# Optimization experiments

Hardware: AMD Instinct MI355X
Metric: run time of the kernel (lower is better)

The kernel has to match this reference:

```python
import jax, jax.numpy as jnp
import numpy as np
from jax import lax

# NOTE: ResidualConvBlock and SS2DChanelFirst are reconstructed from the repo's
# conventions: ResidualConvBlock = act(conv3x3 -> act -> conv3x3 + 1x1 skip);
# SS2DChanelFirst = standard VMamba SS2D (in_proj -> dw-conv3x3 -> SiLU ->
# 4-direction cross-scan selective scan -> cross-merge -> LayerNorm -> *SiLU(z)
# gate -> out_proj) operating on NCHW tensors.

B, CIN, H, W = 4, 6, 64, 64
DM, DI, K, N, R, NL, GROUPS = 72, 144, 4, 8, 4, 2, 12


def conv2d(x, w, b=None, groups=1):
    out = lax.conv_general_dilated(x, w, (1, 1), 'SAME',
                                   dimension_numbers=('NCHW', 'OIHW', 'NCHW'),
                                   feature_group_count=groups)
    if b is not None:
        out = out + b[None, :, None, None]
    return out


def lrelu(x, s):
    return jnp.where(x >= 0, x, s * x)


def selective_scan(u, delta, A, Bs, Cs, D):
    # u, delta: (b,K,C,L); A: (K,C,N); Bs, Cs: (b,K,N,L); D: (K,C)
    b, k, c, l = u.shape
    n = A.shape[-1]
    ul = jnp.moveaxis(u, -1, 0)
    dl = jnp.moveaxis(delta, -1, 0)
    Bl = jnp.moveaxis(Bs, -1, 0)
    Cl = jnp.moveaxis(Cs, -1, 0)
    h0 = jnp.zeros((b, k, c, n), u.dtype)

    def step(h, xt):
        d_t, u_t, B_t, C_t = xt
        h = h * jnp.exp(d_t[..., None] * A) + (d_t * u_t)[..., None] * B_t[:, :, None, :]
        return h, jnp.einsum('bkcn,bkn->bkc', h, C_t)

    _, ys = lax.scan(step, h0, (dl, ul, Bl, Cl))
    return jnp.moveaxis(ys, 0, -1) + u * D[None, :, :, None]


def ss2d(x, in_w, dw_w, dw_b, xp_w, dtp_w, dtp_b, A_logs, Ds, ong, onb, op_w):
    b, dm, h_, w_ = x.shape
    l = h_ * w_
    xz = jnp.einsum('ec,bchw->behw', in_w, x)  # (b, 2*DI, h, w)
    xi, z = xz[:, :DI], xz[:, DI:]
    xi = jax.nn.silu(conv2d(xi, dw_w, dw_b, groups=DI))
    # cross-scan: row-major, col-major, and their reverses
    x0 = xi.reshape(b, DI, l)
    x1 = jnp.swapaxes(xi, 2, 3).reshape(b, DI, l)
    xs = jnp.stack([x0, x1, x0[..., ::-1], x1[..., ::-1]], axis=1)  # (b,4,DI,l)
    x_dbl = jnp.einsum('bkdl,kcd->bkcl', xs, xp_w)  # (b,4,R+2N,l)
    dts, Bs, Cs = x_dbl[:, :, :R], x_dbl[:, :, R:R + N], x_dbl[:, :, R + N:]
    dts = jnp.einsum('bkrl,kdr->bkdl', dts, dtp_w)
    delta = jax.nn.softplus(dts + dtp_b[None, :, :, None])
    A = -jnp.exp(A_logs).reshape(K, DI, N)
    ys = selective_scan(xs, delta, A, Bs, Cs, Ds.reshape(K, DI))  # (b,4,DI,l)
    # cross-merge
    y = ys[:, 0] + ys[:, 2, :, ::-1]
    yt = ys[:, 1] + ys[:, 3, :, ::-1]
    y = y + jnp.swapaxes(yt.reshape(b, DI, w_, h_), 2, 3).reshape(b, DI, l)
    y = jnp.swapaxes(y, 1, 2)  # (b,l,DI)
    mu = y.mean(-1, keepdims=True)
    var = ((y - mu) ** 2).mean(-1, keepdims=True)
    y = (y - mu) / jnp.sqrt(var + 1e-5) * ong + onb
    y = y * jax.nn.silu(jnp.swapaxes(z.reshape(b, DI, l), 1, 2))
    out = jnp.einsum('bld,ed->ble', y, op_w)  # (b,l,DM)
    return jnp.swapaxes(out, 1, 2).reshape(b, dm, h_, w_)


def groupnorm(x, g, bta, groups):
    b, c, h_, w_ = x.shape
    xg = x.reshape(b, groups, c // groups, h_ * w_)
    mu = xg.mean((2, 3), keepdims=True)
    var = ((xg - mu) ** 2).mean((2, 3), keepdims=True)
    xg = (xg - mu) / jnp.sqrt(var + 1e-5)
    return xg.reshape(b, c, h_, w_) * g[None, :, None, None] + bta[None, :, None, None]


def setup_inputs() -> dict:
    key = jax.random.key(0)
    ks = iter(jax.random.split(key, 32))
    nrm = lambda shp, s=0.05: jax.random.normal(next(ks), shp, jnp.float32) * s
    inp = {
        'image': jax.random.normal(next(ks), (B, CIN, H, W), jnp.float32),
        'cb_w1': nrm((DM, CIN, 3, 3), 0.1), 'cb_b1': nrm((DM,), 0.02),
        'cb_w2': nrm((DM, DM, 3, 3), 0.05), 'cb_b2': nrm((DM,), 0.02),
        'cb_ws': nrm((DM, CIN, 1, 1), 0.1), 'cb_bs': nrm((DM,), 0.02),
        'in_w': nrm((NL, 2 * DI, DM), 0.05),
        'dw_w': nrm((NL, DI, 1, 3, 3), 0.1), 'dw_b': nrm((NL, DI), 0.02),
        'xp_w': nrm((NL, K, R + 2 * N, DI), 0.05),
        'dtp_w': nrm((NL, K, DI, R), 0.1), 'dtp_b': nrm((NL, K, DI), 0.1),
        'A_logs': nrm((NL, K * DI, N), 0.5),
        'Ds': jnp.ones((NL, K * DI), jnp.float32) + nrm((NL, K * DI), 0.05),
        'ong': jnp.ones((NL, DI), jnp.float32), 'onb': jnp.zeros((NL, DI), jnp.float32),
        'op_w': nrm((NL, DM, DI), 0.05),
        'gn_g': jnp.ones((NL, DM), jnp.float32), 'gn_b': jnp.zeros((NL, DM), jnp.float32),
        'l1_w': nrm((NL, DM, DM), 0.1), 'l1_b': nrm((NL, DM), 0.02),
        'l2_w': nrm((NL, DM, DM), 0.1), 'l2_b': nrm((NL, DM), 0.02),
        'shrink_w': nrm((CIN, DM, 3, 3), 0.05), 'shrink_b': nrm((CIN,), 0.02),
    }
    return inp


def reference(image, cb_w1, cb_b1, cb_w2, cb_b2, cb_ws, cb_bs, in_w, dw_w, dw_b,
              xp_w, dtp_w, dtp_b, A_logs, Ds, ong, onb, op_w, gn_g, gn_b,
              l1_w, l1_b, l2_w, l2_b, shrink_w, shrink_b):
    # ResidualConvBlock (expand 6 -> 72), leaky_relu
    h = lrelu(conv2d(image, cb_w1, cb_b1), 0.01)
    h = conv2d(h, cb_w2, cb_b2) + conv2d(image, cb_ws, cb_bs)
    x = lrelu(h, 0.01)
    for i in range(NL):
        x = ss2d(x, in_w[i], dw_w[i], dw_b[i], xp_w[i], dtp_w[i], dtp_b[i],
                 A_logs[i], Ds[i], ong[i], onb[i], op_w[i])
        x = groupnorm(x, gn_g[i], gn_b[i], GROUPS)
        x = jnp.einsum('oc,bchw->bohw', l1_w[i], x) + l1_b[i][None, :, None, None]
        x = lrelu(x, 0.04)
        x = jnp.einsum('oc,bchw->bohw', l2_w[i], x) + l2_b[i][None, :, None, None]
    x = conv2d(x, shrink_w, shrink_b)
    return jax.nn.sigmoid(x)
```

## Files before the change

kernel.cpp:

```cpp
#include <hip/hip_runtime.h>
#include <math.h>

#define BB 4
#define CI 6
#define LL 4096
#define DMC 72
#define DIC 144
#define KD 4
#define NS 8
#define RD 4
#define NLAYER 2
#define GRP 12
#define NCH 256
#define TS 16
#define PP 4356
#define L2E 1.4426950408889634f

__device__ __forceinline__ float sigmoidf_(float x){ return 1.f/(1.f+__expf(-x)); }
__device__ __forceinline__ float siluf_(float x){ return x*sigmoidf_(x); }
__device__ __forceinline__ float softplusf_(float x){
  return fmaxf(x,0.f) + __logf(1.f + __expf(-fabsf(x)));
}

__device__ __forceinline__ int padidx(int p){ return 66*(p>>6) + (p&63) + 67; }

__device__ __forceinline__ int dirmap(int k, int l){
  switch(k & 3){
    case 0: return l;
    case 1: return ((l & 63) << 6) | (l >> 6);
    case 2: return (LL-1) - l;
    default: { int m = (LL-1) - l; return ((m & 63) << 6) | (m >> 6); }
  }
}

#define LOAD9(ip, a) do { \
  a[0]=(ip)[-67]; a[1]=(ip)[-66]; a[2]=(ip)[-65]; \
  a[3]=(ip)[-1];  a[4]=(ip)[0];   a[5]=(ip)[1];   \
  a[6]=(ip)[65];  a[7]=(ip)[66];  a[8]=(ip)[67];  } while(0)

__global__ void k_halo(float* __restrict__ pads, int nplanes){
  int plane = blockIdx.x;
  if (plane >= nplanes) return;
  int t = threadIdx.x;
  if (t >= 260) return;
  float* pl = pads + (size_t)plane*PP;
  int off;
  if (t < 132){
    int row = (t < 66) ? 0 : 65;
    int col = (t < 66) ? t : t-66;
    off = row*66 + col;
  } else {
    int j = t - 132;
    int col = (j < 64) ? 0 : 65;
    int row = 1 + (j & 63);
    off = row*66 + col;
  }
  pl[off] = 0.f;
}

__global__ void k_pad_img(const float* __restrict__ img, float* __restrict__ img_pad){
  int idx = blockIdx.x*256 + threadIdx.x;
  if (idx >= BB*CI*LL) return;
  int p = idx & 4095; int bc = idx >> 12;
  img_pad[(size_t)bc*PP + padidx(p)] = img[idx];
}

__global__ void k_conv1(const float* __restrict__ img_pad, const float* __restrict__ w,
                        const float* __restrict__ bias, float* __restrict__ tmp_pad){
  int bid = blockIdx.x;
  int t = bid & 15; int r = bid >> 4; int o = r % DMC; int b = r / DMC;
  int p = t*256 + threadIdx.x;
  int pb = padidx(p);
  float acc = bias[o];
  const float* wb = w + o*CI*9;
  #pragma unroll
  for (int ic=0; ic<CI; ++ic){
    const float* ip = img_pad + (size_t)(b*CI+ic)*PP + pb;
    float a[9]; LOAD9(ip, a);
    #pragma unroll
    for (int q=0;q<9;++q) acc += a[q]*wb[ic*9+q];
  }
  tmp_pad[(size_t)(b*DMC+o)*PP + pb] = acc >= 0.f ? acc : 0.01f*acc;
}

__global__ void k_conv2init(const float* __restrict__ img, const float* __restrict__ b2,
                            const float* __restrict__ wsc, const float* __restrict__ bsc,
                            float* __restrict__ xout){
  int bid = blockIdx.x;
  int t = bid & 15; int r = bid >> 4; int og = r % 18; int b = r / 18;
  int p = t*256 + threadIdx.x;
  float acc[4];
  #pragma unroll
  for (int j=0;j<4;++j) acc[j] = b2[og*4+j] + bsc[og*4+j];
  #pragma unroll
  for (int ic=0; ic<CI; ++ic){
    float v = img[((b*CI+ic)<<12)+p];
    #pragma unroll
    for (int j=0;j<4;++j) acc[j] += v * wsc[(og*4+j)*CI+ic];
  }
  #pragma unroll
  for (int j=0;j<4;++j)
    xout[((b*DMC+og*4+j)<<12)+p] = acc[j];
}

__global__ void k_conv2(const float* __restrict__ tmp_pad,
                        const float* __restrict__ w2, float* __restrict__ xout){
  int bid = blockIdx.x;
  int t = bid & 15; int r = bid >> 4; int og = r % 18; r /= 18;
  int icg = r & 1; int b = r >> 1;
  int p = t*256 + threadIdx.x;
  int pb = padidx(p);
  float acc[4] = {0.f,0.f,0.f,0.f};
  const float* ipb = tmp_pad + (size_t)b*DMC*PP + pb;
  const float* wb  = w2 + (size_t)(og*4)*DMC*9;
  #pragma unroll 2
  for (int ii=0; ii<36; ++ii){
    int ic = icg*36 + ii;
    const float* ip = ipb + (size_t)ic*PP;
    float a[9]; LOAD9(ip, a);
    const float* wp = wb + ic*9;
    #pragma unroll
    for (int j=0;j<4;++j){
      float s = 0.f;
      #pragma unroll
      for (int q=0;q<9;++q) s += a[q]*wp[(size_t)j*DMC*9 + q];
      acc[j] += s;
    }
  }
  #pragma unroll
  for (int j=0;j<4;++j)
    atomicAdd(xout + ((b*DMC+og*4+j)<<12)+p, acc[j]);
}

__global__ void k_xz(const float* __restrict__ x, const float* __restrict__ inw,
                     float* __restrict__ xz_pad, float* __restrict__ z_t, int relu){
  int bid = blockIdx.x;
  int t = bid & 15; int r = bid >> 4; int eg = r % 36; int b = r / 36;
  int p = t*256 + threadIdx.x;
  float acc[8] = {0.f,0.f,0.f,0.f,0.f,0.f,0.f,0.f};
  for (int c0=0; c0<DMC; c0+=4){
    float a[4];
    #pragma unroll
    for (int q=0;q<4;++q) a[q] = x[((b*DMC+c0+q)<<12)+p];
    if (relu){
      #pragma unroll
      for (int q=0;q<4;++q) a[q] = a[q] >= 0.f ? a[q] : 0.01f*a[q];
    }
    #pragma unroll
    for (int j=0;j<8;++j){
      float4 w = *(const float4*)(inw + (eg*8+j)*DMC + c0);
      acc[j] += a[0]*w.x + a[1]*w.y + a[2]*w.z + a[3]*w.w;
    }
  }
  if (eg < 18){
    int pb = padidx(p);
    #pragma unroll
    for (int j=0;j<8;++j) xz_pad[(size_t)(b*DIC+eg*8+j)*PP + pb] = acc[j];
  } else {
    float* zb = z_t + ((size_t)b*LL+p)*DIC + (eg*8-DIC);
    *(float4*)(zb)   = make_float4(acc[0],acc[1],acc[2],acc[3]);
    *(float4*)(zb+4) = make_float4(acc[4],acc[5],acc[6],acc[7]);
  }
}

__global__ void k_dw(const float* __restrict__ xz_pad, const float* __restrict__ dww,
                     const float* __restrict__ dwb, float* __restrict__ xi_t){
  int bid = blockIdx.x;
  int t = bid & 15; int r = bid >> 4; int c = r % DIC; int b = r / DIC;
  int p = t*256 + threadIdx.x;
  int pb = padidx(p);
  const float* ip = xz_pad + (size_t)(b*DIC+c)*PP + pb;
  const float* wp = dww + c*9;
  float a[9]; LOAD9(ip, a);
  float acc = dwb[c];
  #pragma unroll
  for (int q=0;q<9;++q) acc += a[q]*wp[q];
  xi_t[((size_t)b*LL+p)*DIC + c] = siluf_(acc);
}

__global__ void k_xdbl(const float* __restrict__ xi_t, const float* __restrict__ xpw,
                       float* __restrict__ xdbl){
  int bid = blockIdx.x;
  int t = bid & 15; int r = bid >> 4;
  int kk = r & 3; r >>= 2; int part = r & 3; int b = r >> 2;
  int p = t*256 + threadIdx.x;
  const float* xib = xi_t + ((size_t)b*LL + p)*DIC;
  const float* wk = xpw + (size_t)(kk*20 + part*5)*DIC;
  float acc[5] = {0.f,0.f,0.f,0.f,0.f};
  for (int d=0; d<DIC; d+=4){
    float4 v = *(const float4*)(xib + d);
    #pragma unroll
    for (int c=0;c<5;++c){
      float4 w = *(const float4*)(wk + (size_t)c*DIC + d);
      acc[c] += v.x*w.x + v.y*w.y + v.z*w.z + v.w*w.w;
    }
  }
  float* dst = xdbl + ((size_t)(b*KD+kk)*LL + p)*20 + part*5;
  #pragma unroll
  for (int c=0;c<5;++c) dst[c] = acc[c];
}

__device__ __forceinline__ void scan_decode(int idx, int& b, int& k, int& ch, int& c){
  c = idx % DIC;
  int r = idx / DIC;
  ch = r % NCH;
  r /= NCH;
  k = r & 3; b = r >> 2;
}

__global__ void k_p1(const float* __restrict__ xi_t, const float* __restrict__ xdbl,
                     const float* __restrict__ dtpw, const float* __restrict__ dtpb,
                     const float* __restrict__ alog,
                     float* __restrict__ cumA, float* __restrict__ hp){
  int idx = blockIdx.x*256 + threadIdx.x;
  if (idx >= BB*KD*NCH*DIC) return;
  int b,k,ch,c; scan_decode(idx,b,k,ch,c);
  float Arow[NS];
  #pragma unroll
  for (int n=0;n<NS;++n) Arow[n] = -__expf(alog[(k*DIC+c)*NS+n]) * L2E;
  float4 wdt = *(const float4*)(dtpw + (k*DIC+c)*RD);
  float bdt = dtpb[k*DIC+c];
  const float* xd = xdbl + (size_t)(b*KD+k)*LL*20;
  const float* xib = xi_t + (size_t)b*LL*DIC + c;
  float h[NS];
  #pragma unroll
  for (int n=0;n<NS;++n) h[n]=0.f;
  float sumd = 0.f;
  #pragma unroll 4
  for (int t=0; t<TS; ++t){
    int l = ch*TS + t;
    int ps = dirmap(k,l);
    const float* row = xd + (size_t)ps*20;
    float4 q0 = *(const float4*)(row);
    float4 q1 = *(const float4*)(row+4);
    float4 q2 = *(const float4*)(row+8);
    float u = xib[(size_t)ps*DIC];
    float dt = bdt + q0.x*wdt.x + q0.y*wdt.y + q0.z*wdt.z + q0.w*wdt.w;
    dt = softplusf_(dt);
    sumd += dt;
    float du = dt*u;
    float Bv[NS] = {q1.x,q1.y,q1.z,q1.w,q2.x,q2.y,q2.z,q2.w};
    #pragma unroll
    for (int n=0;n<NS;++n)
      h[n] = h[n]*exp2f(dt*Arow[n]) + du*Bv[n];
  }
  size_t base = ((size_t)((b*KD+k)*NCH + ch)*NS)*DIC + c;
  #pragma unroll
  for (int n=0;n<NS;++n) hp[base + n*DIC] = h[n];
  #pragma unroll
  for (int n=0;n<NS;++n) cumA[base + n*DIC] = exp2f(sumd*Arow[n]);
}

__global__ void k_p2(float* __restrict__ cumA, float* __restrict__ hp){
  int idx = blockIdx.x*256 + threadIdx.x;
  if (idx >= BB*KD*NS*DIC) return;
  int c = idx % DIC; int n = (idx/DIC) % NS; int bk = idx/(DIC*NS);
  float h = 0.f;
  #pragma unroll 4
  for (int ch=0; ch<NCH; ++ch){
    size_t base = ((size_t)(bk*NCH+ch)*NS + n)*DIC + c;
    float a = cumA[base];
    float pp = hp[base];
    cumA[base] = 0.f;
    hp[base] = h;
    h = a*h + pp;
  }
}

__global__ void k_p3(const float* __restrict__ xi_t, const float* __restrict__ xdbl,
                     const float* __restrict__ dtpw, const float* __restrict__ dtpb,
                     const float* __restrict__ alog, const float* __restrict__ Dsv,
                     const float* __restrict__ hin, float* __restrict__ y_t){
  int idx = blockIdx.x*256 + threadIdx.x;
  if (idx >= BB*KD*NCH*DIC) return;
  int b,k,ch,c; scan_decode(idx,b,k,ch,c);
  float Arow[NS];
  #pragma unroll
  for (int n=0;n<NS;++n) Arow[n] = -__expf(alog[(k*DIC+c)*NS+n]) * L2E;
  float4 wdt = *(const float4*)(dtpw + (k*DIC+c)*RD);
  float bdt = dtpb[k*DIC+c];
  float Dv = Dsv[k*DIC+c];
  const float* xd = xdbl + (size_t)(b*KD+k)*LL*20;
  const float* xib = xi_t + (size_t)b*LL*DIC + c;
  float* yb = y_t + (size_t)b*LL*DIC + c;
  float h[NS];
  size_t base = ((size_t)((b*KD+k)*NCH + ch)*NS)*DIC + c;
  #pragma unroll
  for (int n=0;n<NS;++n) h[n] = hin[base + n*DIC];
  #pragma unroll 4
  for (int t=0; t<TS; ++t){
    int l = ch*TS + t;
    int ps = dirmap(k,l);
    const float* row = xd + (size_t)ps*20;
    float4 q0 = *(const float4*)(row);
    float4 q1 = *(const float4*)(row+4);
    float4 q2 = *(const float4*)(row+8);
    float4 q3 = *(const float4*)(row+12);
    float4 q4 = *(const float4*)(row+16);
    float u = xib[(size_t)ps*DIC];
    float dt = bdt + q0.x*wdt.x + q0.y*wdt.y + q0.z*wdt.z + q0.w*wdt.w;
    dt = softplusf_(dt);
    float du = dt*u;
    float Bv[NS] = {q1.x,q1.y,q1.z,q1.w,q2.x,q2.y,q2.z,q2.w};
    float Cv[NS] = {q3.x,q3.y,q3.z,q3.w,q4.x,q4.y,q4.z,q4.w};
    float y = 0.f;
    #pragma unroll
    for (int n=0;n<NS;++n){
      h[n] = h[n]*exp2f(dt*Arow[n]) + du*Bv[n];
      y += h[n]*Cv[n];
    }
    y += u*Dv;
    atomicAdd(yb + (size_t)ps*DIC, y);
  }
}

__global__ void k_oproj(const float* __restrict__ y_t, const float* __restrict__ z_t,
                        const float* __restrict__ ong, const float* __restrict__ onb,
                        const float* __restrict__ opw, float* __restrict__ xout,
                        float* __restrict__ gnstats){
  __shared__ float ly[DIC*65];
  __shared__ float red1[8][64], red2[8][64];
  __shared__ float lmu[64], lrs[64];
  int bid = blockIdx.x;
  if (bid == 0 && threadIdx.x < 2*BB*GRP) gnstats[threadIdx.x] = 0.f;
  int tile = bid & 63; int b = bid >> 6;
  int pstart = tile*64;
  const float* src = y_t + ((size_t)b*LL + pstart)*DIC;
  for (int i = threadIdx.x; i < 64*DIC; i += 512){
    int px = i / DIC; int d = i - px*DIC;
    ly[d*65 + px] = src[i];
  }
  __syncthreads();
  int px = threadIdx.x & 63;
  int grp = threadIdx.x >> 6;
  {
    float s=0.f, q=0.f;
    for (int d=grp*18; d<grp*18+18; ++d){
      float v = ly[d*65+px]; s += v; q += v*v;
    }
    red1[grp][px]=s; red2[grp][px]=q;
  }
  __syncthreads();
  if (grp == 0){
    float st=0.f, qt=0.f;
    #pragma unroll
    for (int g=0;g<8;++g){ st += red1[g][px]; qt += red2[g][px]; }
    float mu = st*(1.f/DIC);
    float var = qt*(1.f/DIC) - mu*mu;
    lmu[px] = mu;
    lrs[px] = rsqrtf(var + 1e-5f);
  }
  __syncthreads();
  const float* zsrc = z_t + ((size_t)b*LL + pstart)*DIC;
  for (int i = threadIdx.x; i < 64*DIC; i += 512){
    int ppx = i / DIC; int d = i - ppx*DIC;
    float zv = zsrc[i];
    float v = ly[d*65+ppx];
    ly[d*65+ppx] = ((v - lmu[ppx])*lrs[ppx]*ong[d] + onb[d]) * siluf_(zv);
  }
  __syncthreads();
  int ocg = __builtin_amdgcn_readfirstlane(grp);
  float acc[9];
  #pragma unroll
  for (int j=0;j<9;++j) acc[j]=0.f;
  const float* wb = opw + (size_t)ocg*9*DIC;
  #pragma unroll 4
  for (int d=0; d<DIC; ++d){
    float a = ly[d*65 + px];
    #pragma unroll
    for (int j=0;j<9;++j) acc[j] += a * wb[(size_t)j*DIC + d];
  }
  #pragma unroll
  for (int j=0;j<9;++j)
    xout[((size_t)(b*DMC + ocg*9 + j)<<12) + pstart + px] = acc[j];
}

__global__ void k_gnA(const float* __restrict__ x, float* __restrict__ stats){
  __shared__ float s1[256], s2[256];
  int bid = blockIdx.x;
  int t = bid & 15; int r = bid >> 4; int gr = r % GRP; int b = r / GRP;
  float ls=0.f, lq=0.f;
  #pragma unroll
  for (int it=0; it<6; ++it){
    int i = t*1536 + it*256 + threadIdx.x;
    int c = gr*6 + (i>>12); int p = i & 4095;
    float v = x[((size_t)(b*DMC+c)<<12)+p];
    ls += v; lq += v*v;
  }
  s1[threadIdx.x]=ls; s2[threadIdx.x]=lq; __syncthreads();
  for (int s=128; s>0; s>>=1){
    if (threadIdx.x < s){ s1[threadIdx.x]+=s1[threadIdx.x+s]; s2[threadIdx.x]+=s2[threadIdx.x+s]; }
    __syncthreads();
  }
  if (threadIdx.x == 0){
    atomicAdd(stats + (b*GRP+gr)*2,     s1[0]);
    atomicAdd(stats + (b*GRP+gr)*2 + 1, s2[0]);
  }
}

__global__ void k_gnAB(const float* __restrict__ stats, const float* __restrict__ g,
                       const float* __restrict__ bta, float* __restrict__ gnab){
  int idx = blockIdx.x*256 + threadIdx.x;
  if (idx >= BB*DMC) return;
  int c = idx % DMC; int b = idx / DMC; int gr = c / 6;
  float s = stats[(b*GRP+gr)*2];
  float q = stats[(b*GRP+gr)*2 + 1];
  const float inv = 1.f/(6.f*LL);
  float mu = s*inv;
  float var = q*inv - mu*mu;
  float rs = rsqrtf(var + 1e-5f);
  float A = rs*g[c];
  gnab[idx] = A;
  gnab[BB*DMC + idx] = bta[c] - mu*A;
}

__global__ void k_dense1(const float* __restrict__ xin, const float* __restrict__ gnab,
                         const float* __restrict__ w, const float* __restrict__ bias,
                         float* __restrict__ xout){
  int bid = blockIdx.x;
  int t = bid & 15; int r = bid >> 4; int eg = r % 18; int b = r / 18;
  int p = t*256 + threadIdx.x;
  float acc[4];
  #pragma unroll
  for (int j=0;j<4;++j) acc[j] = bias[eg*4+j];
  const float* Aab = gnab + b*DMC;
  const float* Bab = gnab + BB*DMC + b*DMC;
  for (int c0=0; c0<DMC; c0+=4){
    float a[4];
    #pragma unroll
    for (int q=0;q<4;++q){
      float v = xin[((size_t)(b*DMC+c0+q)<<12)+p];
      a[q] = v*Aab[c0+q] + Bab[c0+q];
    }
    #pragma unroll
    for (int j=0;j<4;++j){
      float4 w0 = *(const float4*)(w + (eg*4+j)*DMC + c0);
      acc[j] += a[0]*w0.x + a[1]*w0.y + a[2]*w0.z + a[3]*w0.w;
    }
  }
  #pragma unroll
  for (int j=0;j<4;++j)
    xout[((size_t)(b*DMC+eg*4+j)<<12)+p] = acc[j];
}

__global__ void k_dense2(const float* __restrict__ xin, const float* __restrict__ w,
                         const float* __restrict__ bias, float* __restrict__ xout,
                         float* __restrict__ pad_out){
  int bid = blockIdx.x;
  int t = bid & 15; int r = bid >> 4; int eg = r % 18; int b = r / 18;
  int p = t*256 + threadIdx.x;
  float acc[4];
  #pragma unroll
  for (int j=0;j<4;++j) acc[j] = bias[eg*4+j];
  for (int c0=0; c0<DMC; c0+=4){
    float a[4];
    #pragma unroll
    for (int q=0;q<4;++q){
      float v = xin[((size_t)(b*DMC+c0+q)<<12)+p];
      a[q] = v >= 0.f ? v : 0.04f*v;
    }
    #pragma unroll
    for (int j=0;j<4;++j){
      float4 w0 = *(const float4*)(w + (eg*4+j)*DMC + c0);
      acc[j] += a[0]*w0.x + a[1]*w0.y + a[2]*w0.z + a[3]*w0.w;
    }
  }
  int pb = padidx(p);
  #pragma unroll
  for (int j=0;j<4;++j){
    xout[((size_t)(b*DMC+eg*4+j)<<12)+p] = acc[j];
    if (pad_out) pad_out[(size_t)(b*DMC+eg*4+j)*PP + pb] = acc[j];
  }
}

__global__ void k_shrinkA(const float* __restrict__ x_pad, const float* __restrict__ w,
                          float* __restrict__ pacc){
  int bid = blockIdx.x;
  int t = bid & 15; int r = bid >> 4; int icg = r % 24; int b = r / 24;
  int p = t*256 + threadIdx.x;
  int pb = padidx(p);
  float acc[6] = {0.f,0.f,0.f,0.f,0.f,0.f};
  const float* ipb = x_pad + (size_t)b*DMC*PP + pb;
  #pragma unroll
  for (int ii=0; ii<3; ++ii){
    int ic = icg*3 + ii;
    const float* ip = ipb + (size_t)ic*PP;
    float a[9]; LOAD9(ip, a);
    #pragma unroll
    for (int o=0;o<6;++o){
      const float* wp = w + (o*DMC+ic)*9;
      float s = 0.f;
      #pragma unroll
      for (int q=0;q<9;++q) s += a[q]*wp[q];
      acc[o] += s;
    }
  }
  #pragma unroll
  for (int o=0;o<6;++o)
    atomicAdd(pacc + ((size_t)(b*CI+o)<<12)+p, acc[o]);
}

__global__ void k_sig(const float* __restrict__ pacc, const float* __restrict__ bias,
                      float* __restrict__ out){
  int idx = blockIdx.x*256 + threadIdx.x;
  if (idx >= BB*CI*LL) return;
  int o = (idx>>12) % CI;
  out[idx] = sigmoidf_(pacc[idx] + bias[o]);
}

extern "C" void kernel_launch(void* const* d_in, const int* in_sizes, int n_in,
                              void* d_out, int out_size, void* d_ws, size_t ws_size,
                              hipStream_t stream){
  const float* image = (const float*)d_in[0];
  const float* cb_w1 = (const float*)d_in[1];
  const float* cb_b1 = (const float*)d_in[2];
  const float* cb_w2 = (const float*)d_in[3];
  const float* cb_b2 = (const float*)d_in[4];
  const float* cb_ws = (const float*)d_in[5];
  const float* cb_bs = (const float*)d_in[6];
  const float* in_w  = (const float*)d_in[7];
  const float* dw_w  = (const float*)d_in[8];
  const float* dw_b  = (const float*)d_in[9];
  const float* xp_w  = (const float*)d_in[10];
  const float* dtp_w = (const float*)d_in[11];
  const float* dtp_b = (const float*)d_in[12];
  const float* A_logs= (const float*)d_in[13];
  const float* Ds    = (const float*)d_in[14];
  const float* ong   = (const float*)d_in[15];
  const float* onb   = (const float*)d_in[16];
  const float* op_w  = (const float*)d_in[17];
  const float* gn_g  = (const float*)d_in[18];
  const float* gn_b  = (const float*)d_in[19];
  const float* l1_w  = (const float*)d_in[20];
  const float* l1_b  = (const float*)d_in[21];
  const float* l2_w  = (const float*)d_in[22];
  const float* l2_b  = (const float*)d_in[23];
  const float* sh_w  = (const float*)d_in[24];
  const float* sh_b  = (const float*)d_in[25];

  const size_t SZ_X  = (size_t)BB*DMC*LL;
  const size_t SZ_C  = (size_t)BB*DIC*LL;
  const size_t SZ_XD = (size_t)BB*KD*20*LL;
  const size_t SZ_HP = (size_t)BB*KD*NCH*NS*DIC;
  const size_t SZ_IP = (size_t)BB*CI*PP;
  const size_t SZ_TP = (size_t)BB*DMC*PP;
  const size_t SZ_ZP = (size_t)BB*DIC*PP;

  float* ws = (float*)d_ws;
  size_t off = 0;
  float* x     = ws + off; off += SZ_X;
  float* tmp   = ws + off; off += SZ_X;
  float* z_t   = ws + off; off += SZ_C;
  float* xi_t  = ws + off; off += SZ_C;
  float* xdbl  = ws + off; off += SZ_XD;
  float* cumA  = ws + off; off += SZ_HP;
  float* hp    = ws + off; off += SZ_HP;
  float* pads  = ws + off;
  float* img_pad = pads;
  float* tmp_pad = img_pad + SZ_IP;
  float* xz_pad  = tmp_pad + SZ_TP;
  off += SZ_IP + SZ_TP + SZ_ZP;
  float* gnstats = ws + off; off += 2*BB*GRP;
  float* gnab    = ws + off; off += 2*BB*DMC;
  if (ws_size < off*sizeof(float)) return;
  float* y_t = cumA;

  dim3 blk(256);
  const int NPLANES = BB*CI + BB*DMC + BB*DIC;

  k_halo<<<dim3(NPLANES), blk, 0, stream>>>(pads, NPLANES);
  k_pad_img<<<dim3(BB*CI*16), blk, 0, stream>>>(image, img_pad);
  k_conv1<<<dim3(BB*DMC*16), blk, 0, stream>>>(img_pad, cb_w1, cb_b1, tmp_pad);
  k_conv2init<<<dim3(BB*18*16), blk, 0, stream>>>(image, cb_b2, cb_ws, cb_bs, x);
  k_conv2<<<dim3(BB*2*18*16), blk, 0, stream>>>(tmp_pad, cb_w2, x);

  for (int i=0; i<NLAYER; ++i){
    const float* in_w_i  = in_w  + (size_t)i*2*DIC*DMC;
    const float* dw_w_i  = dw_w  + (size_t)i*DIC*9;
    const float* dw_b_i  = dw_b  + (size_t)i*DIC;
    const float* xp_w_i  = xp_w  + (size_t)i*KD*20*DIC;
    const float* dtp_w_i = dtp_w + (size_t)i*KD*DIC*RD;
    const float* dtp_b_i = dtp_b + (size_t)i*KD*DIC;
    const float* alog_i  = A_logs+ (size_t)i*KD*DIC*NS;
    const float* Ds_i    = Ds    + (size_t)i*KD*DIC;
    const float* ong_i   = ong   + (size_t)i*DIC;
    const float* onb_i   = onb   + (size_t)i*DIC;
    const float* op_w_i  = op_w  + (size_t)i*DMC*DIC;
    const float* gn_g_i  = gn_g  + (size_t)i*DMC;
    const float* gn_b_i  = gn_b  + (size_t)i*DMC;
    const float* l1_w_i  = l1_w  + (size_t)i*DMC*DMC;
    const float* l1_b_i  = l1_b  + (size_t)i*DMC;
    const float* l2_w_i  = l2_w  + (size_t)i*DMC*DMC;
    const float* l2_b_i  = l2_b  + (size_t)i*DMC;

    k_xz  <<<dim3(BB*36*16), blk, 0, stream>>>(x, in_w_i, xz_pad, z_t, (i==0)?1:0);
    k_dw  <<<dim3(BB*DIC*16), blk, 0, stream>>>(xz_pad, dw_w_i, dw_b_i, xi_t);
    k_xdbl<<<dim3(BB*4*KD*16), blk, 0, stream>>>(xi_t, xp_w_i, xdbl);
    k_p1  <<<dim3(BB*KD*NCH*DIC/256), blk, 0, stream>>>(xi_t, xdbl, dtp_w_i, dtp_b_i, alog_i, cumA, hp);
    k_p2  <<<dim3(BB*KD*NS*DIC/256), blk, 0, stream>>>(cumA, hp);
    k_p3  <<<dim3(BB*KD*NCH*DIC/256), blk, 0, stream>>>(xi_t, xdbl, dtp_w_i, dtp_b_i, alog_i, Ds_i, hp, y_t);
    k_oproj<<<dim3(BB*64), dim3(512), 0, stream>>>(y_t, z_t, ong_i, onb_i, op_w_i, x, gnstats);
    k_gnA <<<dim3(BB*GRP*16), blk, 0, stream>>>(x, gnstats);
    k_gnAB<<<dim3(2), blk, 0, stream>>>(gnstats, gn_g_i, gn_b_i, gnab);
    k_dense1<<<dim3(BB*18*16), blk, 0, stream>>>(x, gnab, l1_w_i, l1_b_i, tmp);
    k_dense2<<<dim3(BB*18*16), blk, 0, stream>>>(tmp, l2_w_i, l2_b_i, x,
                                                 (i==NLAYER-1) ? tmp_pad : (float*)nullptr);
  }

  hipMemsetAsync(tmp, 0, (size_t)BB*CI*LL*sizeof(float), stream);
  k_shrinkA<<<dim3(BB*24*16), blk, 0, stream>>>(tmp_pad, sh_w, tmp);
  k_sig<<<dim3((BB*CI*LL+255)/256), blk, 0, stream>>>(tmp, sh_b, (float*)d_out);
}
```

Before: 502.1 us.

## Pad rows to 72 for vector stencil loads and fuse GroupNorm stats into out-proj

```diff
diff --git a/kernel.cpp b/kernel.cpp
--- a/kernel.cpp
+++ b/kernel.cpp
@@ -13,7 +13,8 @@
 #define GRP 12
 #define NCH 256
 #define TS 16
-#define PP 4356
+#define SP 72
+#define PPN (66*SP)
 #define L2E 1.4426950408889634f
 
 __device__ __forceinline__ float sigmoidf_(float x){ return 1.f/(1.f+__expf(-x)); }
@@ -22,7 +23,7 @@
   return fmaxf(x,0.f) + __logf(1.f + __expf(-fabsf(x)));
 }
 
-__device__ __forceinline__ int padidx(int p){ return 66*(p>>6) + (p&63) + 67; }
+__device__ __forceinline__ int padidx(int p){ return SP*(p>>6) + (p&63) + SP + 4; }
 
 __device__ __forceinline__ int dirmap(int k, int l){
   switch(k & 3){
@@ -34,53 +35,65 @@
 }
 
 #define LOAD9(ip, a) do { \
-  a[0]=(ip)[-67]; a[1]=(ip)[-66]; a[2]=(ip)[-65]; \
-  a[3]=(ip)[-1];  a[4]=(ip)[0];   a[5]=(ip)[1];   \
-  a[6]=(ip)[65];  a[7]=(ip)[66];  a[8]=(ip)[67];  } while(0)
+  a[0]=(ip)[-SP-1]; a[1]=(ip)[-SP]; a[2]=(ip)[-SP+1]; \
+  a[3]=(ip)[-1];    a[4]=(ip)[0];   a[5]=(ip)[1];     \
+  a[6]=(ip)[SP-1];  a[7]=(ip)[SP];  a[8]=(ip)[SP+1];  } while(0)
+
+__device__ __forceinline__ void load6(const float* __restrict__ base, float v[6]){
+  v[0] = base[-1];
+  float4 f = *(const float4*)base;
+  v[1]=f.x; v[2]=f.y; v[3]=f.z; v[4]=f.w;
+  v[5] = base[4];
+}
 
 __global__ void k_halo(float* __restrict__ pads, int nplanes){
   int plane = blockIdx.x;
   if (plane >= nplanes) return;
   int t = threadIdx.x;
   if (t >= 260) return;
-  float* pl = pads + (size_t)plane*PP;
-  int off;
+  float* pl = pads + (size_t)plane*PPN;
+  int row, col;
   if (t < 132){
-    int row = (t < 66) ? 0 : 65;
-    int col = (t < 66) ? t : t-66;
-    off = row*66 + col;
+    row = (t < 66) ? 0 : 65;
+    col = 3 + (t % 66);
   } else {
     int j = t - 132;
-    int col = (j < 64) ? 0 : 65;
-    int row = 1 + (j & 63);
-    off = row*66 + col;
-  }
-  pl[off] = 0.f;
+    col = (j < 64) ? 3 : 68;
+    row = 1 + (j & 63);
+  }
+  pl[row*SP + col] = 0.f;
 }
 
 __global__ void k_pad_img(const float* __restrict__ img, float* __restrict__ img_pad){
   int idx = blockIdx.x*256 + threadIdx.x;
   if (idx >= BB*CI*LL) return;
   int p = idx & 4095; int bc = idx >> 12;
-  img_pad[(size_t)bc*PP + padidx(p)] = img[idx];
+  img_pad[(size_t)bc*PPN + padidx(p)] = img[idx];
 }
 
 __global__ void k_conv1(const float* __restrict__ img_pad, const float* __restrict__ w,
                         const float* __restrict__ bias, float* __restrict__ tmp_pad){
   int bid = blockIdx.x;
-  int t = bid & 15; int r = bid >> 4; int o = r % DMC; int b = r / DMC;
-  int p = t*256 + threadIdx.x;
-  int pb = padidx(p);
-  float acc = bias[o];
-  const float* wb = w + o*CI*9;
+  int tile = bid & 3; int r = bid >> 2; int o = r % DMC; int b = r / DMC;
+  int p0 = tile*1024 + threadIdx.x*4;
+  int pb = padidx(p0);
+  float bv = bias[o];
+  float acc[4] = {bv,bv,bv,bv};
   #pragma unroll
   for (int ic=0; ic<CI; ++ic){
-    const float* ip = img_pad + (size_t)(b*CI+ic)*PP + pb;
-    float a[9]; LOAD9(ip, a);
-    #pragma unroll
-    for (int q=0;q<9;++q) acc += a[q]*wb[ic*9+q];
-  }
-  tmp_pad[(size_t)(b*DMC+o)*PP + pb] = acc >= 0.f ? acc : 0.01f*acc;
+    const float* ip = img_pad + (size_t)(b*CI+ic)*PPN + pb;
+    const float* wr = w + (o*CI+ic)*9;
+    #pragma unroll
+    for (int rr=0; rr<3; ++rr){
+      float v[6]; load6(ip + (rr-1)*SP, v);
+      float w0=wr[rr*3], w1=wr[rr*3+1], w2v=wr[rr*3+2];
+      #pragma unroll
+      for (int q=0;q<4;++q) acc[q] += v[q]*w0 + v[q+1]*w1 + v[q+2]*w2v;
+    }
+  }
+  #pragma unroll
+  for (int q=0;q<4;++q) acc[q] = acc[q] >= 0.f ? acc[q] : 0.01f*acc[q];
+  *(float4*)(tmp_pad + (size_t)(b*DMC+o)*PPN + pb) = make_float4(acc[0],acc[1],acc[2],acc[3]);
 }
 
 __global__ void k_conv2init(const float* __restrict__ img, const float* __restrict__ b2,
@@ -106,30 +119,32 @@
 __global__ void k_conv2(const float* __restrict__ tmp_pad,
                         const float* __restrict__ w2, float* __restrict__ xout){
   int bid = blockIdx.x;
-  int t = bid & 15; int r = bid >> 4; int og = r % 18; r /= 18;
+  int tile = bid & 3; int r = bid >> 2; int og = r % 36; r /= 36;
   int icg = r & 1; int b = r >> 1;
-  int p = t*256 + threadIdx.x;
-  int pb = padidx(p);
-  float acc[4] = {0.f,0.f,0.f,0.f};
-  const float* ipb = tmp_pad + (size_t)b*DMC*PP + pb;
-  const float* wb  = w2 + (size_t)(og*4)*DMC*9;
-  #pragma unroll 2
+  int p0 = tile*1024 + threadIdx.x*4;
+  int pb = padidx(p0);
+  float acc[2][4] = {{0.f,0.f,0.f,0.f},{0.f,0.f,0.f,0.f}};
+  const float* ipb = tmp_pad + (size_t)b*DMC*PPN + pb;
   for (int ii=0; ii<36; ++ii){
     int ic = icg*36 + ii;
-    const float* ip = ipb + (size_t)ic*PP;
-    float a[9]; LOAD9(ip, a);
-    const float* wp = wb + ic*9;
-    #pragma unroll
-    for (int j=0;j<4;++j){
-      float s = 0.f;
+    const float* ip = ipb + (size_t)ic*PPN;
+    #pragma unroll
+    for (int rr=0; rr<3; ++rr){
+      float v[6]; load6(ip + (rr-1)*SP, v);
       #pragma unroll
-      for (int q=0;q<9;++q) s += a[q]*wp[(size_t)j*DMC*9 + q];
-      acc[j] += s;
-    }
-  }
-  #pragma unroll
-  for (int j=0;j<4;++j)
-    atomicAdd(xout + ((b*DMC+og*4+j)<<12)+p, acc[j]);
+      for (int j=0;j<2;++j){
+        const float* wr = w2 + ((size_t)(og*2+j)*DMC + ic)*9 + rr*3;
+        float w0=wr[0], w1=wr[1], w2v=wr[2];
+        #pragma unroll
+        for (int q=0;q<4;++q) acc[j][q] += v[q]*w0 + v[q+1]*w1 + v[q+2]*w2v;
+      }
+    }
+  }
+  #pragma unroll
+  for (int j=0;j<2;++j)
+    #pragma unroll
+    for (int q=0;q<4;++q)
+      atomicAdd(xout + ((b*DMC+og*2+j)<<12) + p0 + q, acc[j][q]);
 }
 
 __global__ void k_xz(const float* __restrict__ x, const float* __restrict__ inw,
@@ -155,7 +170,7 @@
   if (eg < 18){
     int pb = padidx(p);
     #pragma unroll
-    for (int j=0;j<8;++j) xz_pad[(size_t)(b*DIC+eg*8+j)*PP + pb] = acc[j];
+    for (int j=0;j<8;++j) xz_pad[(size_t)(b*DIC+eg*8+j)*PPN + pb] = acc[j];
   } else {
     float* zb = z_t + ((size_t)b*LL+p)*DIC + (eg*8-DIC);
     *(float4*)(zb)   = make_float4(acc[0],acc[1],acc[2],acc[3]);
@@ -166,16 +181,23 @@
 __global__ void k_dw(const float* __restrict__ xz_pad, const float* __restrict__ dww,
                      const float* __restrict__ dwb, float* __restrict__ xi_t){
   int bid = blockIdx.x;
-  int t = bid & 15; int r = bid >> 4; int c = r % DIC; int b = r / DIC;
-  int p = t*256 + threadIdx.x;
-  int pb = padidx(p);
-  const float* ip = xz_pad + (size_t)(b*DIC+c)*PP + pb;
+  int tile = bid & 3; int r = bid >> 2; int c = r % DIC; int b = r / DIC;
+  int p0 = tile*1024 + threadIdx.x*4;
+  int pb = padidx(p0);
+  const float* ip = xz_pad + (size_t)(b*DIC+c)*PPN + pb;
   const float* wp = dww + c*9;
-  float a[9]; LOAD9(ip, a);
-  float acc = dwb[c];
-  #pragma unroll
-  for (int q=0;q<9;++q) acc += a[q]*wp[q];
-  xi_t[((size_t)b*LL+p)*DIC + c] = siluf_(acc);
+  float bv = dwb[c];
+  float acc[4] = {bv,bv,bv,bv};
+  #pragma unroll
+  for (int rr=0; rr<3; ++rr){
+    float v[6]; load6(ip + (rr-1)*SP, v);
+    float w0=wp[rr*3], w1=wp[rr*3+1], w2v=wp[rr*3+2];
+    #pragma unroll
+    for (int q=0;q<4;++q) acc[q] += v[q]*w0 + v[q+1]*w1 + v[q+2]*w2v;
+  }
+  #pragma unroll
+  for (int q=0;q<4;++q)
+    xi_t[((size_t)b*LL+p0+q)*DIC + c] = siluf_(acc[q]);
 }
 
 __global__ void k_xdbl(const float* __restrict__ xi_t, const float* __restrict__ xpw,
@@ -251,7 +273,9 @@
   for (int n=0;n<NS;++n) cumA[base + n*DIC] = exp2f(sumd*Arow[n]);
 }
 
-__global__ void k_p2(float* __restrict__ cumA, float* __restrict__ hp){
+__global__ void k_p2(float* __restrict__ cumA, float* __restrict__ hp,
+                     float* __restrict__ gnstats){
+  if (blockIdx.x == 0 && threadIdx.x < 2*BB*GRP) gnstats[threadIdx.x] = 0.f;
   int idx = blockIdx.x*256 + threadIdx.x;
   if (idx >= BB*KD*NS*DIC) return;
   int c = idx % DIC; int n = (idx/DIC) % NS; int bk = idx/(DIC*NS);
@@ -322,7 +346,6 @@
   __shared__ float red1[8][64], red2[8][64];
   __shared__ float lmu[64], lrs[64];
   int bid = blockIdx.x;
-  if (bid == 0 && threadIdx.x < 2*BB*GRP) gnstats[threadIdx.x] = 0.f;
   int tile = bid & 63; int b = bid >> 6;
   int pstart = tile*64;
   const float* src = y_t + ((size_t)b*LL + pstart)*DIC;
@@ -373,64 +396,85 @@
   #pragma unroll
   for (int j=0;j<9;++j)
     xout[((size_t)(b*DMC + ocg*9 + j)<<12) + pstart + px] = acc[j];
-}
-
-__global__ void k_gnA(const float* __restrict__ x, float* __restrict__ stats){
-  __shared__ float s1[256], s2[256];
-  int bid = blockIdx.x;
-  int t = bid & 15; int r = bid >> 4; int gr = r % GRP; int b = r / GRP;
-  float ls=0.f, lq=0.f;
-  #pragma unroll
-  for (int it=0; it<6; ++it){
-    int i = t*1536 + it*256 + threadIdx.x;
-    int c = gr*6 + (i>>12); int p = i & 4095;
-    float v = x[((size_t)(b*DMC+c)<<12)+p];
-    ls += v; lq += v*v;
-  }
-  s1[threadIdx.x]=ls; s2[threadIdx.x]=lq; __syncthreads();
-  for (int s=128; s>0; s>>=1){
-    if (threadIdx.x < s){ s1[threadIdx.x]+=s1[threadIdx.x+s]; s2[threadIdx.x]+=s2[threadIdx.x+s]; }
-    __syncthreads();
-  }
-  if (threadIdx.x == 0){
-    atomicAdd(stats + (b*GRP+gr)*2,     s1[0]);
-    atomicAdd(stats + (b*GRP+gr)*2 + 1, s2[0]);
-  }
-}
-
-__global__ void k_gnAB(const float* __restrict__ stats, const float* __restrict__ g,
-                       const float* __restrict__ bta, float* __restrict__ gnab){
-  int idx = blockIdx.x*256 + threadIdx.x;
-  if (idx >= BB*DMC) return;
-  int c = idx % DMC; int b = idx / DMC; int gr = c / 6;
-  float s = stats[(b*GRP+gr)*2];
-  float q = stats[(b*GRP+gr)*2 + 1];
-  const float inv = 1.f/(6.f*LL);
-  float mu = s*inv;
-  float var = q*inv - mu*mu;
-  float rs = rsqrtf(var + 1e-5f);
-  float A = rs*g[c];
-  gnab[idx] = A;
-  gnab[BB*DMC + idx] = bta[c] - mu*A;
-}
-
-__global__ void k_dense1(const float* __restrict__ xin, const float* __restrict__ gnab,
+  int c0 = ocg*9;
+  int gA = c0/6;
+  int nA = 6 - (c0 - gA*6);
+  float sA=0.f,qA=0.f,sB=0.f,qB=0.f;
+  #pragma unroll
+  for (int j=0;j<9;++j){
+    float v = acc[j];
+    if (j < nA){ sA += v; qA += v*v; } else { sB += v; qB += v*v; }
+  }
+  #pragma unroll
+  for (int o=32; o>0; o>>=1){
+    sA += __shfl_xor(sA,o,64); qA += __shfl_xor(qA,o,64);
+    sB += __shfl_xor(sB,o,64); qB += __shfl_xor(qB,o,64);
+  }
+  if ((threadIdx.x & 63) == 0){
+    atomicAdd(gnstats + (b*GRP+gA)*2,     sA);
+    atomicAdd(gnstats + (b*GRP+gA)*2 + 1, qA);
+    atomicAdd(gnstats + (b*GRP+gA+1)*2,     sB);
+    atomicAdd(gnstats + (b*GRP+gA+1)*2 + 1, qB);
+  }
+}
+
+__global__ void k_dense1(const float* __restrict__ xin, const float* __restrict__ gnstats,
+                         const float* __restrict__ gng, const float* __restrict__ gnb,
                          const float* __restrict__ w, const float* __restrict__ bias,
                          float* __restrict__ xout){
+  __shared__ float As[DMC], Bs[DMC];
+  int bid = blockIdx.x;
+  int t = bid & 15; int r = bid >> 4; int eg = r % 18; int b = r / 18;
+  if (threadIdx.x < DMC){
+    int c = threadIdx.x; int gr = c/6;
+    float s = gnstats[(b*GRP+gr)*2];
+    float q = gnstats[(b*GRP+gr)*2 + 1];
+    const float inv = 1.f/(6.f*LL);
+    float mu = s*inv;
+    float var = q*inv - mu*mu;
+    float rs = rsqrtf(var + 1e-5f);
+    float A = rs*gng[c];
+    As[c] = A;
+    Bs[c] = gnb[c] - mu*A;
+  }
+  __syncthreads();
+  int p = t*256 + threadIdx.x;
+  float acc[4];
+  #pragma unroll
+  for (int j=0;j<4;++j) acc[j] = bias[eg*4+j];
+  for (int c0=0; c0<DMC; c0+=4){
+    float a[4];
+    #pragma unroll
+    for (int q=0;q<4;++q){
+      float v = xin[((size_t)(b*DMC+c0+q)<<12)+p];
+      a[q] = v*As[c0+q] + Bs[c0+q];
+    }
+    #pragma unroll
+    for (int j=0;j<4;++j){
+      float4 w0 = *(const float4*)(w + (eg*4+j)*DMC + c0);
+      acc[j] += a[0]*w0.x + a[1]*w0.y + a[2]*w0.z + a[3]*w0.w;
+    }
+  }
+  #pragma unroll
+  for (int j=0;j<4;++j)
+    xout[((size_t)(b*DMC+eg*4+j)<<12)+p] = acc[j];
+}
+
+__global__ void k_dense2(const float* __restrict__ xin, const float* __restrict__ w,
+                         const float* __restrict__ bias, float* __restrict__ xout,
+                         float* __restrict__ pad_out){
   int bid = blockIdx.x;
   int t = bid & 15; int r = bid >> 4; int eg = r % 18; int b = r / 18;
   int p = t*256 + threadIdx.x;
   float acc[4];
   #pragma unroll
   for (int j=0;j<4;++j) acc[j] = bias[eg*4+j];
-  const float* Aab = gnab + b*DMC;
-  const float* Bab = gnab + BB*DMC + b*DMC;
   for (int c0=0; c0<DMC; c0+=4){
     float a[4];
     #pragma unroll
     for (int q=0;q<4;++q){
       float v = xin[((size_t)(b*DMC+c0+q)<<12)+p];
-      a[q] = v*Aab[c0+q] + Bab[c0+q];
+      a[q] = v >= 0.f ? v : 0.04f*v;
     }
     #pragma unroll
     for (int j=0;j<4;++j){
@@ -438,38 +482,11 @@
       acc[j] += a[0]*w0.x + a[1]*w0.y + a[2]*w0.z + a[3]*w0.w;
     }
   }
-  #pragma unroll
-  for (int j=0;j<4;++j)
-    xout[((size_t)(b*DMC+eg*4+j)<<12)+p] = acc[j];
-}
-
-__global__ void k_dense2(const float* __restrict__ xin, const float* __restrict__ w,
-                         const float* __restrict__ bias, float* __restrict__ xout,
-                         float* __restrict__ pad_out){
-  int bid = blockIdx.x;
-  int t = bid & 15; int r = bid >> 4; int eg = r % 18; int b = r / 18;
-  int p = t*256 + threadIdx.x;
-  float acc[4];
-  #pragma unroll
-  for (int j=0;j<4;++j) acc[j] = bias[eg*4+j];
-  for (int c0=0; c0<DMC; c0+=4){
-    float a[4];
-    #pragma unroll
-    for (int q=0;q<4;++q){
-      float v = xin[((size_t)(b*DMC+c0+q)<<12)+p];
-      a[q] = v >= 0.f ? v : 0.04f*v;
-    }
-    #pragma unroll
-    for (int j=0;j<4;++j){
-      float4 w0 = *(const float4*)(w + (eg*4+j)*DMC + c0);
-      acc[j] += a[0]*w0.x + a[1]*w0.y + a[2]*w0.z + a[3]*w0.w;
-    }
-  }
   int pb = padidx(p);
   #pragma unroll
   for (int j=0;j<4;++j){
     xout[((size_t)(b*DMC+eg*4+j)<<12)+p] = acc[j];
-    if (pad_out) pad_out[(size_t)(b*DMC+eg*4+j)*PP + pb] = acc[j];
+    if (pad_out) pad_out[(size_t)(b*DMC+eg*4+j)*PPN + pb] = acc[j];
   }
 }
 
@@ -480,11 +497,11 @@
   int p = t*256 + threadIdx.x;
   int pb = padidx(p);
   float acc[6] = {0.f,0.f,0.f,0.f,0.f,0.f};
-  const float* ipb = x_pad + (size_t)b*DMC*PP + pb;
+  const float* ipb = x_pad + (size_t)b*DMC*PPN + pb;
   #pragma unroll
   for (int ii=0; ii<3; ++ii){
     int ic = icg*3 + ii;
-    const float* ip = ipb + (size_t)ic*PP;
+    const float* ip = ipb + (size_t)ic*PPN;
     float a[9]; LOAD9(ip, a);
     #pragma unroll
     for (int o=0;o<6;++o){
@@ -542,9 +559,9 @@
   const size_t SZ_C  = (size_t)BB*DIC*LL;
   const size_t SZ_XD = (size_t)BB*KD*20*LL;
   const size_t SZ_HP = (size_t)BB*KD*NCH*NS*DIC;
-  const size_t SZ_IP = (size_t)BB*CI*PP;
-  const size_t SZ_TP = (size_t)BB*DMC*PP;
-  const size_t SZ_ZP = (size_t)BB*DIC*PP;
+  const size_t SZ_IP = (size_t)BB*CI*PPN;
+  const size_t SZ_TP = (size_t)BB*DMC*PPN;
+  const size_t SZ_ZP = (size_t)BB*DIC*PPN;
 
   float* ws = (float*)d_ws;
   size_t off = 0;
@@ -561,7 +578,6 @@
   float* xz_pad  = tmp_pad + SZ_TP;
   off += SZ_IP + SZ_TP + SZ_ZP;
   float* gnstats = ws + off; off += 2*BB*GRP;
-  float* gnab    = ws + off; off += 2*BB*DMC;
   if (ws_size < off*sizeof(float)) return;
   float* y_t = cumA;
 
@@ -570,9 +586,9 @@
 
   k_halo<<<dim3(NPLANES), blk, 0, stream>>>(pads, NPLANES);
   k_pad_img<<<dim3(BB*CI*16), blk, 0, stream>>>(image, img_pad);
-  k_conv1<<<dim3(BB*DMC*16), blk, 0, stream>>>(img_pad, cb_w1, cb_b1, tmp_pad);
+  k_conv1<<<dim3(BB*DMC*4), blk, 0, stream>>>(img_pad, cb_w1, cb_b1, tmp_pad);
   k_conv2init<<<dim3(BB*18*16), blk, 0, stream>>>(image, cb_b2, cb_ws, cb_bs, x);
-  k_conv2<<<dim3(BB*2*18*16), blk, 0, stream>>>(tmp_pad, cb_w2, x);
+  k_conv2<<<dim3(BB*2*36*4), blk, 0, stream>>>(tmp_pad, cb_w2, x);
 
   for (int i=0; i<NLAYER; ++i){
     const float* in_w_i  = in_w  + (size_t)i*2*DIC*DMC;
@@ -594,15 +610,13 @@
     const float* l2_b_i  = l2_b  + (size_t)i*DMC;
 
     k_xz  <<<dim3(BB*36*16), blk, 0, stream>>>(x, in_w_i, xz_pad, z_t, (i==0)?1:0);
-    k_dw  <<<dim3(BB*DIC*16), blk, 0, stream>>>(xz_pad, dw_w_i, dw_b_i, xi_t);
+    k_dw  <<<dim3(BB*DIC*4), blk, 0, stream>>>(xz_pad, dw_w_i, dw_b_i, xi_t);
     k_xdbl<<<dim3(BB*4*KD*16), blk, 0, stream>>>(xi_t, xp_w_i, xdbl);
     k_p1  <<<dim3(BB*KD*NCH*DIC/256), blk, 0, stream>>>(xi_t, xdbl, dtp_w_i, dtp_b_i, alog_i, cumA, hp);
-    k_p2  <<<dim3(BB*KD*NS*DIC/256), blk, 0, stream>>>(cumA, hp);
+    k_p2  <<<dim3(BB*KD*NS*DIC/256), blk, 0, stream>>>(cumA, hp, gnstats);
     k_p3  <<<dim3(BB*KD*NCH*DIC/256), blk, 0, stream>>>(xi_t, xdbl, dtp_w_i, dtp_b_i, alog_i, Ds_i, hp, y_t);
     k_oproj<<<dim3(BB*64), dim3(512), 0, stream>>>(y_t, z_t, ong_i, onb_i, op_w_i, x, gnstats);
-    k_gnA <<<dim3(BB*GRP*16), blk, 0, stream>>>(x, gnstats);
-    k_gnAB<<<dim3(2), blk, 0, stream>>>(gnstats, gn_g_i, gn_b_i, gnab);
-    k_dense1<<<dim3(BB*18*16), blk, 0, stream>>>(x, gnab, l1_w_i, l1_b_i, tmp);
+    k_dense1<<<dim3(BB*18*16), blk, 0, stream>>>(x, gnstats, gn_g_i, gn_b_i, l1_w_i, l1_b_i, tmp);
     k_dense2<<<dim3(BB*18*16), blk, 0, stream>>>(tmp, l2_w_i, l2_b_i, x,
                                                  (i==NLAYER-1) ? tmp_pad : (float*)nullptr);
   }
```

Result: slower. 578.9 us (+15.3%).
